# Kernel tuning notes

Hardware: AMD Instinct MI355X
Metric: run time of the kernel (lower is better)

The kernel has to match this reference:

```python
import jax, jax.numpy as jnp
import numpy as np

NEG_INF = -jnp.inf


def setup_inputs() -> dict:
    B, T, E, H = 16, 1024, 1024, 1024  # batch, seq, embed_dim, head_dim (T <= H required by original buffer slicing)
    key = jax.random.key(0)
    k1, k2, k3, k4, k5, k6 = jax.random.split(key, 6)
    return {
        "key": jax.random.normal(k1, (B, T, E), dtype=jnp.float32),
        "query": jax.random.normal(k2, (B, T, E), dtype=jnp.float32),
        "value": jax.random.normal(k3, (B, T, E), dtype=jnp.float32),
        "padding_mask": jnp.zeros((B, 1, T), dtype=jnp.int32),
        # nn.Linear(embed_dim, head_dim, bias=False) weights: [head_dim, embed_dim]
        "Wk": jax.random.normal(k4, (H, E), dtype=jnp.float32) * (E ** -0.5),
        "Wq": jax.random.normal(k5, (H, E), dtype=jnp.float32) * (E ** -0.5),
        "Wv": jax.random.normal(k6, (H, E), dtype=jnp.float32) * (E ** -0.5),
    }


def reference(key, query, value, padding_mask, Wk, Wq, Wv):
    # key/query/value: [B, T, E]; W*: [H, E]
    B, T, E = key.shape
    k = jnp.einsum("bte,he->bth", key, Wk)
    q = jnp.einsum("bte,he->bth", query, Wq)
    v = jnp.einsum("bte,he->bth", value, Wv)
    # NOTE: original scales by d_k = key.size(-1) = embed_dim, not head_dim
    scale = 1.0 / jnp.sqrt(jnp.float32(E))
    qk = jnp.einsum("bth,bsh->bts", q, k) * scale  # [B, T, T]
    # causal buffer is tril(ones, diagonal=1): position i can attend to j <= i+1
    causal = jnp.tril(jnp.ones((T, T), dtype=jnp.float32), k=1)
    qk = jnp.where(causal == 0, NEG_INF, qk)
    qk = jnp.where(padding_mask == 1, NEG_INF, qk)  # padding_mask broadcasts [B,1,T] -> [B,T,T]
    p = jax.nn.softmax(qk, axis=-1)
    attn = jnp.einsum("bts,bsh->bth", p, v)  # dropout is identity in eval mode
    return attn
```

## Files before the change

kernel.cpp:

```cpp
#include <hip/hip_runtime.h>
#include <hip/hip_bf16.h>
#include <stdint.h>

typedef __bf16 bf16;
typedef __attribute__((ext_vector_type(8))) __bf16 bf16x8;
typedef __attribute__((ext_vector_type(4))) __bf16 bf16x4;
typedef __attribute__((ext_vector_type(4))) float  f32x4;

static __device__ __forceinline__ void gll16(const void* g, void* lds_base) {
  __builtin_amdgcn_global_load_lds((__attribute__((address_space(1))) void*)g,
                                   (__attribute__((address_space(3))) void*)lds_base,
                                   16, 0, 0);
}

#define BARR  __builtin_amdgcn_s_barrier()
#define VMW(N) asm volatile("s_waitcnt vmcnt(" #N ")" ::: "memory")
#define LGKM0 asm volatile("s_waitcnt lgkmcnt(0)" ::: "memory")
#define SB0   __builtin_amdgcn_sched_barrier(0)

template <int VARIANT>
__global__ __launch_bounds__(512, 2) void gemm8(const bf16* __restrict__ a0,
                                                const bf16* __restrict__ a1,
                                                const bf16* __restrict__ a2,
                                                const bf16* __restrict__ b0,
                                                const bf16* __restrict__ b1,
                                                const bf16* __restrict__ b2,
                                                bf16* __restrict__ c0,
                                                bf16* __restrict__ c1,
                                                bf16* __restrict__ c2,
                                                float* __restrict__ Cf,
                                                const int* __restrict__ pad) {
  extern __shared__ char smem[];
  char* ldsA = smem;
  char* ldsB = smem + 32768;

  const int tid = threadIdx.x;
  const int lane = tid & 63, wave = tid >> 6;
  const int lo = lane & 15, hi = lane >> 4;
  const int wmi = wave >> 2, wni = wave & 3;
  const int swz = (lo & 3) << 4;

  const int nwg = gridDim.x;
  const int id = (blockIdx.x % 8) * (nwg >> 3) + blockIdx.x / 8;

  int row0, col0, nt, batch = 0, trans = 0;
  const bf16 *Ap, *Bp;
  bf16* Cb;
  if (VARIANT == 0) {
    const int seg = id >> 8, idl = id & 255;
    row0 = (idl >> 2) * 256; col0 = (idl & 3) * 256; nt = 32;
    trans = (seg == 2);
    const bf16* As = seg == 0 ? a0 : (seg == 1 ? a1 : a2);
    const bf16* Bs = seg == 0 ? b0 : (seg == 1 ? b1 : b2);
    Cb = seg == 0 ? c0 : (seg == 1 ? c1 : c2);
    Ap = As + (size_t)row0 * 1024;
    Bp = Bs + (size_t)col0 * 1024;
  } else {
    batch = id >> 4;
    const int r = id & 15, it = r >> 2, jt = r & 3;
    row0 = it * 256; col0 = jt * 256;
    nt = (VARIANT == 3) ? min(32, 8 * it + 10) : 32;
    if (VARIANT == 2 && jt > it + 1) return;
    if (VARIANT == 2 && jt == it + 1) {
      bf16* Sb = c0 + ((size_t)batch << 20);
      bf16x8 z = {};
#pragma unroll
      for (int q = 0; q < 16; ++q) {
        const int off = (q * 512 + tid) * 8;
        *(bf16x8*)(Sb + (size_t)(row0 + (off >> 8)) * 1024 + col0 + (off & 255)) = z;
      }
      return;
    }
    Ap = a0 + ((size_t)batch << 20) + (size_t)row0 * 1024;
    Bp = b0 + ((size_t)batch << 20) + (size_t)col0 * 1024;
    Cb = c0;
  }
  const int ntm1 = nt - 1;

  auto stg = [&](const bf16* base, char* ldsOp, int tidx, int slot) {
    const int tc = tidx > ntm1 ? ntm1 : tidx;
#pragma unroll
    for (int r = 0; r < 2; ++r) {
      const int x  = wave * 2048 + r * 1024 + lane * 16;
      const int xs = x ^ (((x >> 6) & 3) << 4);
      gll16((const char*)base + (size_t)(xs >> 6) * 2048 + (size_t)tc * 64 + (xs & 63),
            ldsOp + slot * 16384 + wave * 2048 + r * 1024);
    }
  };

  f32x4 acc[8][4] = {};
  bf16x8 af[4], bfr[4];

  auto rdA = [&](int mh, int slot) {
#pragma unroll
    for (int i = 0; i < 4; ++i) {
      const int row = wmi * 128 + mh * 64 + i * 16 + lo;
      af[i] = *(const bf16x8*)(ldsA + slot * 16384 + ((row * 64 + hi * 16) ^ swz));
    }
  };
  auto rdB = [&](int slot) {
#pragma unroll
    for (int n = 0; n < 4; ++n) {
      const int row = wni * 64 + n * 16 + lo;
      bfr[n] = *(const bf16x8*)(ldsB + slot * 16384 + ((row * 64 + hi * 16) ^ swz));
    }
  };
  auto mmaQ = [&](int mh) {
    __builtin_amdgcn_s_setprio(1);
#pragma unroll
    for (int i = 0; i < 4; ++i)
#pragma unroll
      for (int n = 0; n < 4; ++n)
        acc[mh * 4 + i][n] = __builtin_amdgcn_mfma_f32_16x16x32_bf16(
            af[i], bfr[n], acc[mh * 4 + i][n], 0, 0, 0);
    __builtin_amdgcn_s_setprio(0);
  };

  stg(Bp, ldsB, 0, 0);
  stg(Ap, ldsA, 0, 0);
  stg(Bp, ldsB, 1, 1);
  VMW(2);
  BARR;

#pragma unroll 2
  for (int u = 0; u < nt; ++u) {
    const int cur = u & 1;
    rdA(0, cur);
    rdB(cur);
    stg(Ap, ldsA, u + 1, cur ^ 1);
    BARR; LGKM0; SB0;
    mmaQ(0);
    BARR;
    rdA(1, cur);
    stg(Bp, ldsB, u + 2, cur);
    BARR; LGKM0; SB0;
    mmaQ(1);
    VMW(2);
    BARR;
  }

  if (VARIANT == 0) {
    if (!trans) {
#pragma unroll
      for (int m = 0; m < 8; ++m)
#pragma unroll
        for (int n = 0; n < 4; ++n) {
          const int c = col0 + wni * 64 + n * 16 + lo;
          const int rbase = row0 + wmi * 128 + m * 16 + hi * 4;
#pragma unroll
          for (int j = 0; j < 4; ++j)
            Cb[(size_t)(rbase + j) * 1024 + c] = (bf16)acc[m][n][j];
        }
    } else {
#pragma unroll
      for (int m = 0; m < 8; ++m)
#pragma unroll
        for (int n = 0; n < 4; ++n) {
          const int r = row0 + wmi * 128 + m * 16 + hi * 4;
          const int c = col0 + wni * 64 + n * 16 + lo;
          const int bb = r >> 10, tt = r & 1023;
          bf16x4 h = { (bf16)acc[m][n][0], (bf16)acc[m][n][1],
                       (bf16)acc[m][n][2], (bf16)acc[m][n][3] };
          *(bf16x4*)(Cb + ((size_t)bb << 20) + ((size_t)c << 10) + tt) = h;
        }
    }
  } else if (VARIANT == 2) {
    const float NINF = -__builtin_inff();
#pragma unroll
    for (int n = 0; n < 4; ++n) {
      const int s = col0 + wni * 64 + n * 16 + lo;
      const int pd = pad[(batch << 10) + s];
#pragma unroll
      for (int m = 0; m < 8; ++m) {
        const int tbase = row0 + wmi * 128 + m * 16 + hi * 4;
#pragma unroll
        for (int j = 0; j < 4; ++j) {
          float v = acc[m][n][j] * 0.03125f;
          if (s > tbase + j + 1) v = 0.f;
          else if (pd != 0) v = NINF;
          Cb[((size_t)batch << 20) + (size_t)(tbase + j) * 1024 + s] = (bf16)v;
        }
      }
    }
  } else {
#pragma unroll
    for (int m = 0; m < 8; ++m)
#pragma unroll
      for (int n = 0; n < 4; ++n) {
        const int h2 = col0 + wni * 64 + n * 16 + lo;
        const int tbase = row0 + wmi * 128 + m * 16 + hi * 4;
#pragma unroll
        for (int j = 0; j < 4; ++j)
          Cf[((size_t)batch << 20) + (size_t)(tbase + j) * 1024 + h2] = acc[m][n][j];
      }
  }
  asm volatile("s_waitcnt vmcnt(0)" ::: "memory");
}

__global__ __launch_bounds__(256) void cvt3_kernel(const float* __restrict__ s0,
                                                   const float* __restrict__ s1,
                                                   const float* __restrict__ s2,
                                                   bf16* __restrict__ d0,
                                                   bf16* __restrict__ d1,
                                                   bf16* __restrict__ d2) {
  const int seg = blockIdx.x >> 13, blk = blockIdx.x & 8191;
  const float* src = seg == 0 ? s0 : (seg == 1 ? s1 : s2);
  bf16* dst = seg == 0 ? d0 : (seg == 1 ? d1 : d2);
  const int i = (blk * 256 + threadIdx.x) * 8;
  const f32x4 a = *(const f32x4*)(src + i);
  const f32x4 b = *(const f32x4*)(src + i + 4);
  bf16x8 o = { (bf16)a[0], (bf16)a[1], (bf16)a[2], (bf16)a[3],
               (bf16)b[0], (bf16)b[1], (bf16)b[2], (bf16)b[3] };
  *(bf16x8*)(dst + i) = o;
}

__global__ __launch_bounds__(256) void cvtW_kernel(const float* __restrict__ s0,
                                                   const float* __restrict__ s1,
                                                   const float* __restrict__ s2,
                                                   bf16* __restrict__ d0,
                                                   bf16* __restrict__ d1,
                                                   bf16* __restrict__ d2) {
  const int seg = blockIdx.x >> 9, blk = blockIdx.x & 511;
  const float* src = seg == 0 ? s0 : (seg == 1 ? s1 : s2);
  bf16* dst = seg == 0 ? d0 : (seg == 1 ? d1 : d2);
  const int i = (blk * 256 + threadIdx.x) * 8;
  const f32x4 a = *(const f32x4*)(src + i);
  const f32x4 b = *(const f32x4*)(src + i + 4);
  bf16x8 o = { (bf16)a[0], (bf16)a[1], (bf16)a[2], (bf16)a[3],
               (bf16)b[0], (bf16)b[1], (bf16)b[2], (bf16)b[3] };
  *(bf16x8*)(dst + i) = o;
}

__global__ __launch_bounds__(64) void corner_kernel(const bf16* __restrict__ Q,
                                                    const bf16* __restrict__ K,
                                                    const int* __restrict__ pad,
                                                    bf16* __restrict__ S) {
  const int b = blockIdx.x / 3, it = blockIdx.x % 3;
  const int t = it * 256 + 255, s = (it + 1) * 256;
  const int lane = threadIdx.x;
  const bf16* q = Q + ((size_t)b << 20) + (size_t)t * 1024 + lane * 16;
  const bf16* k = K + ((size_t)b << 20) + (size_t)s * 1024 + lane * 16;
  bf16x8 q0 = *(const bf16x8*)q, q1 = *(const bf16x8*)(q + 8);
  bf16x8 k0 = *(const bf16x8*)k, k1 = *(const bf16x8*)(k + 8);
  float d = 0.f;
#pragma unroll
  for (int j = 0; j < 8; ++j) d += (float)q0[j] * (float)k0[j] + (float)q1[j] * (float)k1[j];
#pragma unroll
  for (int o = 32; o; o >>= 1) d += __shfl_xor(d, o, 64);
  if (lane == 0) {
    float v = d * 0.03125f;
    if (pad[(b << 10) + s] != 0) v = -__builtin_inff();
    S[((size_t)b << 20) + (size_t)t * 1024 + s] = (bf16)v;
  }
}

__global__ __launch_bounds__(256) void softmax_kernel(bf16* __restrict__ S) {
  const int row  = blockIdx.x * 4 + (threadIdx.x >> 6);
  const int lane = threadIdx.x & 63;
  const int t = row & 1023;
  const int w = min(1024, t + 2);
  const bool act = lane * 16 < w;
  bf16* r = S + (size_t)row * 1024 + lane * 16;
  bf16x8 v0 = {}, v1 = {};
  float f[16];
#pragma unroll
  for (int j = 0; j < 16; ++j) f[j] = -1e30f;
  if (act) {
    v0 = *(const bf16x8*)r;
    v1 = *(const bf16x8*)(r + 8);
#pragma unroll
    for (int j = 0; j < 16; ++j)
      if (lane * 16 + j < w) f[j] = (float)(j < 8 ? v0[j] : v1[j - 8]);
  }
  float m = f[0];
#pragma unroll
  for (int j = 1; j < 16; ++j) m = fmaxf(m, f[j]);
#pragma unroll
  for (int o = 32; o; o >>= 1) m = fmaxf(m, __shfl_xor(m, o, 64));
  float sum = 0.f;
  float e[16];
#pragma unroll
  for (int j = 0; j < 16; ++j) { e[j] = __expf(f[j] - m); sum += e[j]; }
#pragma unroll
  for (int o = 32; o; o >>= 1) sum += __shfl_xor(sum, o, 64);
  const float inv = 1.0f / sum;
  if (act) {
#pragma unroll
    for (int j = 0; j < 8; ++j) {
      v0[j] = (bf16)(lane * 16 + j < w ? e[j] * inv : 0.f);
      v1[j] = (bf16)(lane * 16 + 8 + j < w ? e[8 + j] * inv : 0.f);
    }
    *(bf16x8*)r = v0;
    *(bf16x8*)(r + 8) = v1;
  }
}

extern "C" void kernel_launch(void* const* d_in, const int* in_sizes, int n_in,
                              void* d_out, int out_size, void* d_ws, size_t ws_size,
                              hipStream_t stream) {
  const float* key   = (const float*)d_in[0];
  const float* query = (const float*)d_in[1];
  const float* value = (const float*)d_in[2];
  const int*   pad   = (const int*)d_in[3];
  const float* Wk    = (const float*)d_in[4];
  const float* Wq    = (const float*)d_in[5];
  const float* Wv    = (const float*)d_in[6];
  float* out = (float*)d_out;

  bf16* Wkb = (bf16*)d_ws;
  bf16* Wqb = Wkb + (1 << 20);
  bf16* Wvb = Wqb + (1 << 20);
  bf16* qb  = Wvb + (1 << 20);
  bf16* kb  = qb  + (16 << 20);
  bf16* vT  = kb  + (16 << 20);
  bf16* S   = vT  + (16 << 20);
  bf16* Xq  = S;
  bf16* Xk  = (bf16*)d_out;
  bf16* Xv  = Xk + (16 << 20);

  hipFuncSetAttribute(reinterpret_cast<const void*>(&gemm8<0>),
                      hipFuncAttributeMaxDynamicSharedMemorySize, 65536);
  hipFuncSetAttribute(reinterpret_cast<const void*>(&gemm8<2>),
                      hipFuncAttributeMaxDynamicSharedMemorySize, 65536);
  hipFuncSetAttribute(reinterpret_cast<const void*>(&gemm8<3>),
                      hipFuncAttributeMaxDynamicSharedMemorySize, 65536);

  cvtW_kernel<<<1536, 256, 0, stream>>>(Wk, Wq, Wv, Wkb, Wqb, Wvb);
  cvt3_kernel<<<24576, 256, 0, stream>>>(query, key, value, Xq, Xk, Xv);

  gemm8<0><<<768, 512, 65536, stream>>>(Xq, Xk, Xv, Wqb, Wkb, Wvb,
                                        qb, kb, vT, nullptr, nullptr);

  gemm8<2><<<256, 512, 65536, stream>>>(qb, nullptr, nullptr, kb, nullptr, nullptr,
                                        S, nullptr, nullptr, nullptr, pad);
  corner_kernel<<<48, 64, 0, stream>>>(qb, kb, pad, S);
  softmax_kernel<<<4096, 256, 0, stream>>>(S);
  gemm8<3><<<256, 512, 65536, stream>>>(S, nullptr, nullptr, vT, nullptr, nullptr,
                                        nullptr, nullptr, nullptr, out, nullptr);
}
```

Baseline: 249.9 us.

## Fold Wq and Wk into one product matrix and skip K projection

The query and key projections are replaced by a precomputed product P = Wq^T·Wk (via transposed weight conversion and a small 16-block GEMM), so Y = Xq·P is used directly against the raw bf16 key input for the scores. This removes one of the three large per-batch projection GEMMs and the storage of q and k, at the cost of a small extra weight GEMM and a transpose kernel. The LDS swizzle pattern is also changed. The reassociation changes rounding, since the product matrix is stored in bf16.

```diff
diff --git a/kernel.cpp b/kernel.cpp
--- a/kernel.cpp
+++ b/kernel.cpp
@@ -21,13 +21,10 @@
 template <int VARIANT>
 __global__ __launch_bounds__(512, 2) void gemm8(const bf16* __restrict__ a0,
                                                 const bf16* __restrict__ a1,
-                                                const bf16* __restrict__ a2,
                                                 const bf16* __restrict__ b0,
                                                 const bf16* __restrict__ b1,
-                                                const bf16* __restrict__ b2,
                                                 bf16* __restrict__ c0,
                                                 bf16* __restrict__ c1,
-                                                bf16* __restrict__ c2,
                                                 float* __restrict__ Cf,
                                                 const int* __restrict__ pad) {
   extern __shared__ char smem[];
@@ -38,7 +35,7 @@
   const int lane = tid & 63, wave = tid >> 6;
   const int lo = lane & 15, hi = lane >> 4;
   const int wmi = wave >> 2, wni = wave & 3;
-  const int swz = (lo & 3) << 4;
+  const int swz = ((lo >> 1) & 3) << 4;
 
   const int nwg = gridDim.x;
   const int id = (blockIdx.x % 8) * (nwg >> 3) + blockIdx.x / 8;
@@ -49,10 +46,10 @@
   if (VARIANT == 0) {
     const int seg = id >> 8, idl = id & 255;
     row0 = (idl >> 2) * 256; col0 = (idl & 3) * 256; nt = 32;
-    trans = (seg == 2);
-    const bf16* As = seg == 0 ? a0 : (seg == 1 ? a1 : a2);
-    const bf16* Bs = seg == 0 ? b0 : (seg == 1 ? b1 : b2);
-    Cb = seg == 0 ? c0 : (seg == 1 ? c1 : c2);
+    trans = seg;
+    const bf16* As = seg ? a1 : a0;
+    const bf16* Bs = seg ? b1 : b0;
+    Cb = seg ? c1 : c0;
     Ap = As + (size_t)row0 * 1024;
     Bp = Bs + (size_t)col0 * 1024;
   } else {
@@ -82,7 +79,7 @@
 #pragma unroll
     for (int r = 0; r < 2; ++r) {
       const int x  = wave * 2048 + r * 1024 + lane * 16;
-      const int xs = x ^ (((x >> 6) & 3) << 4);
+      const int xs = x ^ (((x >> 7) & 3) << 4);
       gll16((const char*)base + (size_t)(xs >> 6) * 2048 + (size_t)tc * 64 + (xs & 63),
             ldsOp + slot * 16384 + wave * 2048 + r * 1024);
     }
@@ -214,33 +211,52 @@
   *(bf16x8*)(dst + i) = o;
 }
 
-__global__ __launch_bounds__(256) void cvtW_kernel(const float* __restrict__ s0,
-                                                   const float* __restrict__ s1,
-                                                   const float* __restrict__ s2,
-                                                   bf16* __restrict__ d0,
-                                                   bf16* __restrict__ d1,
-                                                   bf16* __restrict__ d2) {
-  const int seg = blockIdx.x >> 9, blk = blockIdx.x & 511;
-  const float* src = seg == 0 ? s0 : (seg == 1 ? s1 : s2);
-  bf16* dst = seg == 0 ? d0 : (seg == 1 ? d1 : d2);
-  const int i = (blk * 256 + threadIdx.x) * 8;
-  const f32x4 a = *(const f32x4*)(src + i);
-  const f32x4 b = *(const f32x4*)(src + i + 4);
-  bf16x8 o = { (bf16)a[0], (bf16)a[1], (bf16)a[2], (bf16)a[3],
-               (bf16)b[0], (bf16)b[1], (bf16)b[2], (bf16)b[3] };
-  *(bf16x8*)(dst + i) = o;
-}
-
-__global__ __launch_bounds__(64) void corner_kernel(const bf16* __restrict__ Q,
-                                                    const bf16* __restrict__ K,
+__global__ __launch_bounds__(256) void cvtWT_kernel(const float* __restrict__ Wq,
+                                                    const float* __restrict__ Wk,
+                                                    const float* __restrict__ Wv,
+                                                    bf16* __restrict__ WqT,
+                                                    bf16* __restrict__ WkT,
+                                                    bf16* __restrict__ Wvb) {
+  const int t = threadIdx.x;
+  if (blockIdx.x >= 512) {
+    const int i = ((blockIdx.x - 512) * 256 + t) * 8;
+    const f32x4 a = *(const f32x4*)(Wv + i);
+    const f32x4 b = *(const f32x4*)(Wv + i + 4);
+    bf16x8 o = { (bf16)a[0], (bf16)a[1], (bf16)a[2], (bf16)a[3],
+                 (bf16)b[0], (bf16)b[1], (bf16)b[2], (bf16)b[3] };
+    *(bf16x8*)(Wvb + i) = o;
+    return;
+  }
+  const int m = blockIdx.x >> 8;
+  const float* src = m ? Wk : Wq;
+  bf16* dst = m ? WkT : WqT;
+  const int tile = blockIdx.x & 255;
+  const int tr = (tile >> 4) * 64, tc = (tile & 15) * 64;
+  __shared__ bf16 s[64][72];
+#pragma unroll
+  for (int it = 0; it < 4; ++it) {
+    const int row = it * 16 + (t >> 4), col = (t & 15) * 4;
+    const f32x4 v = *(const f32x4*)(src + (size_t)(tr + row) * 1024 + tc + col);
+#pragma unroll
+    for (int j = 0; j < 4; ++j) s[col + j][row] = (bf16)v[j];
+  }
+  __syncthreads();
+  const int c = t >> 2, rb = (t & 3) * 16;
+  bf16* d = dst + (size_t)(tc + c) * 1024 + tr + rb;
+  *(bf16x8*)(d)     = *(const bf16x8*)&s[c][rb];
+  *(bf16x8*)(d + 8) = *(const bf16x8*)&s[c][rb + 8];
+}
+
+__global__ __launch_bounds__(64) void corner_kernel(const bf16* __restrict__ Y,
+                                                    const bf16* __restrict__ Xk,
                                                     const int* __restrict__ pad,
                                                     bf16* __restrict__ S) {
   const int b = blockIdx.x / 3, it = blockIdx.x % 3;
   const int t = it * 256 + 255, s = (it + 1) * 256;
   const int lane = threadIdx.x;
-  const bf16* q = Q + ((size_t)b << 20) + (size_t)t * 1024 + lane * 16;
-  const bf16* k = K + ((size_t)b << 20) + (size_t)s * 1024 + lane * 16;
-  bf16x8 q0 = *(const bf16x8*)q, q1 = *(const bf16x8*)(q + 8);
+  const bf16* y = Y  + ((size_t)b << 20) + (size_t)t * 1024 + lane * 16;
+  const bf16* k = Xk + ((size_t)b << 20) + (size_t)s * 1024 + lane * 16;
+  bf16x8 q0 = *(const bf16x8*)y, q1 = *(const bf16x8*)(y + 8);
   bf16x8 k0 = *(const bf16x8*)k, k1 = *(const bf16x8*)(k + 8);
   float d = 0.f;
 #pragma unroll
@@ -307,12 +323,12 @@
   const float* Wv    = (const float*)d_in[6];
   float* out = (float*)d_out;
 
-  bf16* Wkb = (bf16*)d_ws;
-  bf16* Wqb = Wkb + (1 << 20);
-  bf16* Wvb = Wqb + (1 << 20);
-  bf16* qb  = Wvb + (1 << 20);
-  bf16* kb  = qb  + (16 << 20);
-  bf16* vT  = kb  + (16 << 20);
+  bf16* WqT = (bf16*)d_ws;
+  bf16* WkT = WqT + (1 << 20);
+  bf16* Wvb = WkT + (1 << 20);
+  bf16* P   = Wvb + (1 << 20);
+  bf16* Y   = P   + (1 << 20);
+  bf16* vT  = Y   + (16 << 20);
   bf16* S   = vT  + (16 << 20);
   bf16* Xq  = S;
   bf16* Xk  = (bf16*)d_out;
@@ -325,16 +341,17 @@
   hipFuncSetAttribute(reinterpret_cast<const void*>(&gemm8<3>),
                       hipFuncAttributeMaxDynamicSharedMemorySize, 65536);
 
-  cvtW_kernel<<<1536, 256, 0, stream>>>(Wk, Wq, Wv, Wkb, Wqb, Wvb);
+  cvtWT_kernel<<<1024, 256, 0, stream>>>(Wq, Wk, Wv, WqT, WkT, Wvb);
+  gemm8<0><<<16, 512, 65536, stream>>>(WkT, nullptr, WqT, nullptr,
+                                       P, nullptr, nullptr, nullptr);
   cvt3_kernel<<<24576, 256, 0, stream>>>(query, key, value, Xq, Xk, Xv);
 
-  gemm8<0><<<768, 512, 65536, stream>>>(Xq, Xk, Xv, Wqb, Wkb, Wvb,
-                                        qb, kb, vT, nullptr, nullptr);
-
-  gemm8<2><<<256, 512, 65536, stream>>>(qb, nullptr, nullptr, kb, nullptr, nullptr,
-                                        S, nullptr, nullptr, nullptr, pad);
-  corner_kernel<<<48, 64, 0, stream>>>(qb, kb, pad, S);
+  gemm8<0><<<512, 512, 65536, stream>>>(Xq, Xv, P, Wvb, Y, vT, nullptr, nullptr);
+
+  gemm8<2><<<256, 512, 65536, stream>>>(Y, nullptr, Xk, nullptr,
+                                        S, nullptr, nullptr, pad);
+  corner_kernel<<<48, 64, 0, stream>>>(Y, Xk, pad, S);
   softmax_kernel<<<4096, 256, 0, stream>>>(S);
-  gemm8<3><<<256, 512, 65536, stream>>>(S, nullptr, nullptr, vT, nullptr, nullptr,
-                                        nullptr, nullptr, nullptr, out, nullptr);
-}
+  gemm8<3><<<256, 512, 65536, stream>>>(S, nullptr, vT, nullptr,
+                                        nullptr, nullptr, out, nullptr);
+}
```

Result: faster. 238.1 us (-4.7%).
